# Optimization experiments

Measured on AMD Instinct MI355X. Metric: run time of the kernel, lower is better.

## Reference

```python
import jax, jax.numpy as jnp
import numpy as np

EPS = 1e-7  # K.epsilon()

def setup_inputs() -> dict:
    key = jax.random.key(0)
    k1, k2, k3 = jax.random.split(key, 3)
    B, T, D = 32, 2048, 512
    x = jax.random.normal(k1, (B, T, D), dtype=jnp.float32)
    W = jax.random.normal(k2, (D, D), dtype=jnp.float32) * (1.0 / np.sqrt(D))
    b = jnp.zeros((D,), dtype=jnp.float32)
    u = jax.random.normal(k3, (D,), dtype=jnp.float32) * (1.0 / np.sqrt(D))
    return {"x": x, "W": W, "b": b, "u": u}

def reference(x, W, b, u):
    # uit = tanh(x @ W + b)  -> [B, T, D]
    uit = jnp.tanh(jnp.einsum('btd,de->bte', x, W) + b)
    # scores: sum over feature dim of uit * u -> [B, T]
    ait = jnp.einsum('btd,d->bt', uit, u)
    # exp + normalize over T (no mask); matches original exp/sum form
    a = jnp.exp(ait)
    a = a / (jnp.sum(a, axis=1, keepdims=True) + EPS)
    # weighted sum pooling over T -> [B, D]
    return jnp.einsum('btd,bt->bd', x, a)
```

## Files before the change

kernel.cpp:

```cpp
#include <hip/hip_runtime.h>
#include <math.h>

#define D_DIM 512

typedef short short8v __attribute__((ext_vector_type(8)));
typedef unsigned short ushort8v __attribute__((ext_vector_type(8)));
typedef float f32x16 __attribute__((ext_vector_type(16)));

__device__ inline unsigned short f2bf(float f) {
    union { float f; unsigned int u; } a; a.f = f;
    unsigned int u = a.u;
    unsigned int r = (u + 0x7fffu + ((u >> 16) & 1u)) >> 16;
    return (unsigned short)r;
}

__device__ inline float fast_tanh(float y) {
    float e2 = __expf(2.f * y);
    return 1.f - __fdividef(2.f, e2 + 1.f);
}

#define ASYNC_CP16(gp, lp) \
    __builtin_amdgcn_global_load_lds( \
        (const __attribute__((address_space(1))) void*)(gp), \
        (__attribute__((address_space(3))) void*)(lp), 16, 0, 0)

__global__ __launch_bounds__(1024) void wt_kernel(const float* __restrict__ W,
                                                  unsigned short* __restrict__ Wb2) {
    __shared__ __align__(16) unsigned short lbuf[16384];
    const int s = blockIdx.x;
    const int tid = threadIdx.x;
    #pragma unroll
    for (int i = 0; i < 4; ++i) {
        int flat = tid + i * 1024;
        int kr = flat >> 7;
        int e4 = (flat & 127) * 4;
        float4 v = *(const float4*)(W + (size_t)(s * 32 + kr) * D_DIM + e4);
        int ks = kr >> 4, half = (kr >> 3) & 1, j = kr & 7;
        float vv[4] = {v.x, v.y, v.z, v.w};
        #pragma unroll
        for (int q = 0; q < 4; ++q) {
            int e = e4 + q, nt = e >> 5, nl = e & 31;
            lbuf[(((nt * 2 + ks) * 2 + half) * 32 + nl) * 8 + j] = f2bf(vv[q]);
        }
    }
    __syncthreads();
    #pragma unroll
    for (int i = 0; i < 2; ++i) {
        int c = tid + i * 1024;
        *(ushort8v*)(Wb2 + (size_t)s * 16384 + c * 8) = *(const ushort8v*)&lbuf[c * 8];
    }
}

constexpr int XLDE = 40;

__global__ __launch_bounds__(512, 2) void gemm_ait_mfma(
    const float* __restrict__ x, const unsigned short* __restrict__ Wb2,
    const float* __restrict__ bias, const float* __restrict__ u,
    float* __restrict__ ait)
{
    __shared__ __align__(16) unsigned short wsh[2][16384];
    __shared__ __align__(16) unsigned short xs[2][128 * XLDE];
    __shared__ float rowpart[4][128];

    const int tid  = threadIdx.x;
    const int wave = tid >> 6;
    const int lane = tid & 63;
    const int half = lane >> 5;
    const int nl   = lane & 31;
    const int wr   = wave >> 2;
    const int wc   = wave & 3;
    const int m0   = blockIdx.x * 128;

    f32x16 acc[2][4];
    #pragma unroll
    for (int mi = 0; mi < 2; ++mi)
        #pragma unroll
        for (int ni = 0; ni < 4; ++ni)
            #pragma unroll
            for (int r = 0; r < 16; ++r) acc[mi][ni][r] = 0.f;

    const int xr = tid >> 2;
    const int xc = tid & 3;
    const float* xbase = x + (size_t)(m0 + xr) * D_DIM + xc * 8;

    #pragma unroll
    for (int i = 0; i < 4; ++i)
        ASYNC_CP16(Wb2 + tid * 8 + i * 4096, &wsh[0][tid * 8 + i * 4096]);
    float4 px0 = *(const float4*)(xbase);
    float4 px1 = *(const float4*)(xbase + 4);

    for (int s = 0; s < 16; ++s) {
        const int pb = s & 1;
        {
            ushort8v pk;
            pk[0] = f2bf(px0.x); pk[1] = f2bf(px0.y); pk[2] = f2bf(px0.z); pk[3] = f2bf(px0.w);
            pk[4] = f2bf(px1.x); pk[5] = f2bf(px1.y); pk[6] = f2bf(px1.z); pk[7] = f2bf(px1.w);
            *(ushort8v*)&xs[pb][xr * XLDE + xc * 8] = pk;
        }
        __syncthreads();

        if (s + 1 < 16) {
            const unsigned short* wsrc = Wb2 + (size_t)(s + 1) * 16384;
            #pragma unroll
            for (int i = 0; i < 4; ++i)
                ASYNC_CP16(wsrc + tid * 8 + i * 4096, &wsh[1 - pb][tid * 8 + i * 4096]);
            px0 = *(const float4*)(xbase + (s + 1) * 32);
            px1 = *(const float4*)(xbase + (s + 1) * 32 + 4);
        }

        #pragma unroll
        for (int ks = 0; ks < 2; ++ks) {
            short8v af[2], bfr[4];
            #pragma unroll
            for (int mi = 0; mi < 2; ++mi)
                af[mi] = *(const short8v*)&xs[pb][(wr * 64 + mi * 32 + nl) * XLDE + ks * 16 + half * 8];
            #pragma unroll
            for (int ni = 0; ni < 4; ++ni)
                bfr[ni] = *(const short8v*)&wsh[pb][(((wc * 4 + ni) * 2 + ks) * 2 + half) * 256 + nl * 8];
            #pragma unroll
            for (int mi = 0; mi < 2; ++mi)
                #pragma unroll
                for (int ni = 0; ni < 4; ++ni)
                    acc[mi][ni] = __builtin_amdgcn_mfma_f32_32x32x16_bf16(
                        af[mi], bfr[ni], acc[mi][ni], 0, 0, 0);
        }
    }

    float rowsum[2][16];
    #pragma unroll
    for (int mi = 0; mi < 2; ++mi)
        #pragma unroll
        for (int r = 0; r < 16; ++r) rowsum[mi][r] = 0.f;

    #pragma unroll
    for (int mi = 0; mi < 2; ++mi) {
        #pragma unroll
        for (int ni = 0; ni < 4; ++ni) {
            int col = wc * 128 + ni * 32 + nl;
            float be = bias[col], ue = u[col];
            #pragma unroll
            for (int r = 0; r < 16; ++r)
                rowsum[mi][r] += fast_tanh(acc[mi][ni][r] + be) * ue;
        }
    }
    #pragma unroll
    for (int mi = 0; mi < 2; ++mi)
        #pragma unroll
        for (int r = 0; r < 16; ++r) {
            float v = rowsum[mi][r];
            v += __shfl_xor(v, 1, 64);
            v += __shfl_xor(v, 2, 64);
            v += __shfl_xor(v, 4, 64);
            v += __shfl_xor(v, 8, 64);
            v += __shfl_xor(v, 16, 64);
            rowsum[mi][r] = v;
        }
    if (nl == 0) {
        #pragma unroll
        for (int mi = 0; mi < 2; ++mi)
            #pragma unroll
            for (int r = 0; r < 16; ++r) {
                int row = wr * 64 + mi * 32 + (r & 3) + 8 * (r >> 2) + 4 * half;
                rowpart[wc][row] = rowsum[mi][r];
            }
    }
    __syncthreads();
    if (tid < 128)
        ait[m0 + tid] = rowpart[0][tid] + rowpart[1][tid] + rowpart[2][tid] + rowpart[3][tid];
}

__global__ __launch_bounds__(256) void gemm_ait_f32(
    const float* __restrict__ x, const float* __restrict__ W,
    const float* __restrict__ bias, const float* __restrict__ u,
    float* __restrict__ ait)
{
    __shared__ float xsf[64][68];
    __shared__ float wshf[64][132];
    const int tid = threadIdx.x;
    const int tx = tid & 15, ty = tid >> 4;
    const int m0 = blockIdx.x * 64;
    float rowsum[4] = {0.f, 0.f, 0.f, 0.f};
    for (int e0 = 0; e0 < D_DIM; e0 += 128) {
        float acc[4][8];
        #pragma unroll
        for (int i = 0; i < 4; ++i)
            #pragma unroll
            for (int j = 0; j < 8; ++j) acc[i][j] = 0.f;
        for (int kc = 0; kc < D_DIM; kc += 64) {
            #pragma unroll
            for (int i = 0; i < 4; ++i) {
                int idx = tid + i * 256;
                int r = idx >> 4, c = (idx & 15) * 4;
                *(float4*)&xsf[r][c] = *(const float4*)(x + (size_t)(m0 + r) * D_DIM + kc + c);
            }
            #pragma unroll
            for (int i = 0; i < 8; ++i) {
                int idx = tid + i * 256;
                int r = idx >> 5, c = (idx & 31) * 4;
                *(float4*)&wshf[r][c] = *(const float4*)(W + (size_t)(kc + r) * D_DIM + e0 + c);
            }
            __syncthreads();
            #pragma unroll 4
            for (int k = 0; k < 64; ++k) {
                float xv[4];
                #pragma unroll
                for (int i = 0; i < 4; ++i) xv[i] = xsf[ty * 4 + i][k];
                float4 w0 = *(const float4*)&wshf[k][tx * 8];
                float4 w1 = *(const float4*)&wshf[k][tx * 8 + 4];
                #pragma unroll
                for (int i = 0; i < 4; ++i) {
                    acc[i][0] += xv[i] * w0.x; acc[i][1] += xv[i] * w0.y;
                    acc[i][2] += xv[i] * w0.z; acc[i][3] += xv[i] * w0.w;
                    acc[i][4] += xv[i] * w1.x; acc[i][5] += xv[i] * w1.y;
                    acc[i][6] += xv[i] * w1.z; acc[i][7] += xv[i] * w1.w;
                }
            }
            __syncthreads();
        }
        #pragma unroll
        for (int j = 0; j < 8; ++j) {
            int e = e0 + tx * 8 + j;
            float be = bias[e], ue = u[e];
            #pragma unroll
            for (int i = 0; i < 4; ++i) rowsum[i] += tanhf(acc[i][j] + be) * ue;
        }
    }
    float* red = &xsf[0][0];
    #pragma unroll
    for (int i = 0; i < 4; ++i) red[(ty * 4 + i) * 16 + tx] = rowsum[i];
    __syncthreads();
    if (tid < 64) {
        float s = 0.f;
        #pragma unroll
        for (int j = 0; j < 16; ++j) s += red[tid * 16 + j];
        ait[m0 + tid] = s;
    }
}

__global__ __launch_bounds__(256) void softmax_kernel(float* __restrict__ ait, int T)
{
    const int b = blockIdx.x;
    float* p = ait + (size_t)b * T;
    const int tid = threadIdx.x;
    float ev[8];
    float local = 0.f;
    #pragma unroll
    for (int i = 0; i < 8; ++i) {
        ev[i] = expf(p[tid + i * 256]);
        local += ev[i];
    }
    #pragma unroll
    for (int off = 32; off > 0; off >>= 1)
        local += __shfl_down(local, off, 64);
    __shared__ float wsum[4];
    const int wv = tid >> 6, lane = tid & 63;
    if (lane == 0) wsum[wv] = local;
    __syncthreads();
    float total = wsum[0] + wsum[1] + wsum[2] + wsum[3];
    float inv = 1.0f / (total + 1e-7f);
    #pragma unroll
    for (int i = 0; i < 8; ++i) p[tid + i * 256] = ev[i] * inv;
}

__global__ __launch_bounds__(256) void pool_partial_kernel(
    const float* __restrict__ x, const float* __restrict__ a,
    float* __restrict__ partial, int T)
{
    const int chunks = T >> 8;
    const int b = blockIdx.x / chunks;
    const int c = blockIdx.x % chunks;
    const int tid = threadIdx.x;
    const int th = tid >> 7;
    const int d = (tid & 127) * 4;

    const float* xp = x + ((size_t)b * T + c * 256) * D_DIM + d;
    const float* ap = a + (size_t)b * T + c * 256;

    float4 acc = {0.f, 0.f, 0.f, 0.f};
    #pragma unroll 8
    for (int t = th; t < 256; t += 2) {
        float s = ap[t];
        float4 xv = *(const float4*)(xp + (size_t)t * D_DIM);
        acc.x += xv.x * s; acc.y += xv.y * s;
        acc.z += xv.z * s; acc.w += xv.w * s;
    }
    __shared__ float4 tmp[128];
    if (th == 1) tmp[tid & 127] = acc;
    __syncthreads();
    if (th == 0) {
        float4 o = tmp[tid];
        acc.x += o.x; acc.y += o.y; acc.z += o.z; acc.w += o.w;
        *(float4*)(partial + (size_t)blockIdx.x * D_DIM + tid * 4) = acc;
    }
}

__global__ __launch_bounds__(256) void pool_reduce_kernel(
    const float* __restrict__ partial, float* __restrict__ out, int chunks)
{
    const int b = blockIdx.x;
    const int tid = threadIdx.x;
    const int d = tid * 2;
    float2 acc = {0.f, 0.f};
    for (int c = 0; c < chunks; ++c) {
        float2 v = *(const float2*)(partial + ((size_t)b * chunks + c) * D_DIM + d);
        acc.x += v.x; acc.y += v.y;
    }
    *(float2*)(out + (size_t)b * D_DIM + d) = acc;
}

__global__ __launch_bounds__(256) void pool_atomic_kernel(
    const float* __restrict__ x, const float* __restrict__ a,
    float* __restrict__ out, int T)
{
    const int chunks = T >> 8;
    const int b = blockIdx.x / chunks;
    const int c = blockIdx.x % chunks;
    const int tid = threadIdx.x;
    const int th = tid >> 7;
    const int d = (tid & 127) * 4;
    const float* xp = x + ((size_t)b * T + c * 256) * D_DIM + d;
    const float* ap = a + (size_t)b * T + c * 256;
    float4 acc = {0.f, 0.f, 0.f, 0.f};
    #pragma unroll 8
    for (int t = th; t < 256; t += 2) {
        float s = ap[t];
        float4 xv = *(const float4*)(xp + (size_t)t * D_DIM);
        acc.x += xv.x * s; acc.y += xv.y * s;
        acc.z += xv.z * s; acc.w += xv.w * s;
    }
    __shared__ float4 tmp[128];
    if (th == 1) tmp[tid & 127] = acc;
    __syncthreads();
    if (th == 0) {
        float4 o = tmp[tid];
        float* op = out + (size_t)b * D_DIM + tid * 4;
        atomicAdd(op + 0, acc.x + o.x);
        atomicAdd(op + 1, acc.y + o.y);
        atomicAdd(op + 2, acc.z + o.z);
        atomicAdd(op + 3, acc.w + o.w);
    }
}

extern "C" void kernel_launch(void* const* d_in, const int* in_sizes, int n_in,
                              void* d_out, int out_size, void* d_ws, size_t ws_size,
                              hipStream_t stream)
{
    const float* x    = (const float*)d_in[0];
    const float* W    = (const float*)d_in[1];
    const float* bias = (const float*)d_in[2];
    const float* u    = (const float*)d_in[3];
    float* out = (float*)d_out;

    const int Dd = in_sizes[2];
    const int M  = in_sizes[0] / Dd;
    const int B  = out_size / Dd;
    const int T  = M / B;
    const int chunks = T >> 8;

    const size_t wb_bytes  = (size_t)Dd * Dd * sizeof(unsigned short);
    const size_t ait_bytes = (size_t)M * sizeof(float);

    if (ws_size >= wb_bytes + ait_bytes) {
        unsigned short* Wb2 = (unsigned short*)d_ws;
        float* ait     = (float*)((char*)d_ws + wb_bytes);
        float* partial = (float*)d_ws;

        wt_kernel<<<dim3(16), dim3(1024), 0, stream>>>(W, Wb2);
        gemm_ait_mfma<<<dim3(M / 128), dim3(512), 0, stream>>>(x, Wb2, bias, u, ait);
        softmax_kernel<<<dim3(B), dim3(256), 0, stream>>>(ait, T);
        pool_partial_kernel<<<dim3(B * chunks), dim3(256), 0, stream>>>(x, ait, partial, T);
        pool_reduce_kernel<<<dim3(B), dim3(256), 0, stream>>>(partial, out, chunks);
    } else {
        float* ait = (float*)d_ws;
        gemm_ait_f32<<<dim3(M / 64), dim3(256), 0, stream>>>(x, W, bias, u, ait);
        softmax_kernel<<<dim3(B), dim3(256), 0, stream>>>(ait, T);
        hipMemsetAsync(d_out, 0, (size_t)out_size * sizeof(float), stream);
        pool_atomic_kernel<<<dim3(B * chunks), dim3(256), 0, stream>>>(x, ait, out, T);
    }
}
```

Measured before the change: 262.4 us.

## Shrink GEMM row tile to 64 and widen pooling blocks to 512 threads

The scoring GEMM now handles 64 rows per block instead of 128, and each of the 8 waves owns a 64-column slice across all rows. The launch bound now asks for 4 blocks per CU, and the grid doubles. The pooling partial kernel uses 512 threads, with four time-strided groups reduced through shared memory, for more memory parallelism. The smaller tile raises occupancy, but every block must still load the full W, so W traffic from LDS and L2 per row doubles.

```diff
diff --git a/kernel.cpp b/kernel.cpp
--- a/kernel.cpp
+++ b/kernel.cpp
@@ -5,6 +5,7 @@
 
 typedef short short8v __attribute__((ext_vector_type(8)));
 typedef unsigned short ushort8v __attribute__((ext_vector_type(8)));
+typedef unsigned short ushort4v __attribute__((ext_vector_type(4)));
 typedef float f32x16 __attribute__((ext_vector_type(16)));
 
 __device__ inline unsigned short f2bf(float f) {
@@ -53,49 +54,46 @@
 
 constexpr int XLDE = 40;
 
-__global__ __launch_bounds__(512, 2) void gemm_ait_mfma(
+__global__ __launch_bounds__(512, 4) void gemm_ait_mfma(
     const float* __restrict__ x, const unsigned short* __restrict__ Wb2,
     const float* __restrict__ bias, const float* __restrict__ u,
     float* __restrict__ ait)
 {
     __shared__ __align__(16) unsigned short wsh[2][16384];
-    __shared__ __align__(16) unsigned short xs[2][128 * XLDE];
-    __shared__ float rowpart[4][128];
+    __shared__ __align__(16) unsigned short xs[2][64 * XLDE];
+    __shared__ float rowpart[8][64];
 
     const int tid  = threadIdx.x;
     const int wave = tid >> 6;
     const int lane = tid & 63;
     const int half = lane >> 5;
     const int nl   = lane & 31;
-    const int wr   = wave >> 2;
-    const int wc   = wave & 3;
-    const int m0   = blockIdx.x * 128;
-
-    f32x16 acc[2][4];
+    const int m0   = blockIdx.x * 64;
+
+    f32x16 acc[2][2];
     #pragma unroll
     for (int mi = 0; mi < 2; ++mi)
         #pragma unroll
-        for (int ni = 0; ni < 4; ++ni)
+        for (int ni = 0; ni < 2; ++ni)
             #pragma unroll
             for (int r = 0; r < 16; ++r) acc[mi][ni][r] = 0.f;
 
-    const int xr = tid >> 2;
-    const int xc = tid & 3;
-    const float* xbase = x + (size_t)(m0 + xr) * D_DIM + xc * 8;
+    const int xr  = tid >> 3;
+    const int xc4 = tid & 7;
+    const float* xbase = x + (size_t)(m0 + xr) * D_DIM + xc4 * 4;
 
     #pragma unroll
     for (int i = 0; i < 4; ++i)
         ASYNC_CP16(Wb2 + tid * 8 + i * 4096, &wsh[0][tid * 8 + i * 4096]);
-    float4 px0 = *(const float4*)(xbase);
-    float4 px1 = *(const float4*)(xbase + 4);
+    float4 px = *(const float4*)(xbase);
 
     for (int s = 0; s < 16; ++s) {
         const int pb = s & 1;
         {
-            ushort8v pk;
-            pk[0] = f2bf(px0.x); pk[1] = f2bf(px0.y); pk[2] = f2bf(px0.z); pk[3] = f2bf(px0.w);
-            pk[4] = f2bf(px1.x); pk[5] = f2bf(px1.y); pk[6] = f2bf(px1.z); pk[7] = f2bf(px1.w);
-            *(ushort8v*)&xs[pb][xr * XLDE + xc * 8] = pk;
+            ushort4v pk;
+            pk[0] = f2bf(px.x); pk[1] = f2bf(px.y);
+            pk[2] = f2bf(px.z); pk[3] = f2bf(px.w);
+            *(ushort4v*)&xs[pb][xr * XLDE + xc4 * 4] = pk;
         }
         __syncthreads();
 
@@ -104,23 +102,22 @@
             #pragma unroll
             for (int i = 0; i < 4; ++i)
                 ASYNC_CP16(wsrc + tid * 8 + i * 4096, &wsh[1 - pb][tid * 8 + i * 4096]);
-            px0 = *(const float4*)(xbase + (s + 1) * 32);
-            px1 = *(const float4*)(xbase + (s + 1) * 32 + 4);
+            px = *(const float4*)(xbase + (s + 1) * 32);
         }
 
         #pragma unroll
         for (int ks = 0; ks < 2; ++ks) {
-            short8v af[2], bfr[4];
+            short8v af[2], bfr[2];
             #pragma unroll
             for (int mi = 0; mi < 2; ++mi)
-                af[mi] = *(const short8v*)&xs[pb][(wr * 64 + mi * 32 + nl) * XLDE + ks * 16 + half * 8];
-            #pragma unroll
-            for (int ni = 0; ni < 4; ++ni)
-                bfr[ni] = *(const short8v*)&wsh[pb][(((wc * 4 + ni) * 2 + ks) * 2 + half) * 256 + nl * 8];
+                af[mi] = *(const short8v*)&xs[pb][(mi * 32 + nl) * XLDE + ks * 16 + half * 8];
+            #pragma unroll
+            for (int ni = 0; ni < 2; ++ni)
+                bfr[ni] = *(const short8v*)&wsh[pb][(((wave * 2 + ni) * 2 + ks) * 2 + half) * 256 + nl * 8];
             #pragma unroll
             for (int mi = 0; mi < 2; ++mi)
                 #pragma unroll
-                for (int ni = 0; ni < 4; ++ni)
+                for (int ni = 0; ni < 2; ++ni)
                     acc[mi][ni] = __builtin_amdgcn_mfma_f32_32x32x16_bf16(
                         af[mi], bfr[ni], acc[mi][ni], 0, 0, 0);
         }
@@ -135,8 +132,8 @@
     #pragma unroll
     for (int mi = 0; mi < 2; ++mi) {
         #pragma unroll
-        for (int ni = 0; ni < 4; ++ni) {
-            int col = wc * 128 + ni * 32 + nl;
+        for (int ni = 0; ni < 2; ++ni) {
+            int col = wave * 64 + ni * 32 + nl;
             float be = bias[col], ue = u[col];
             #pragma unroll
             for (int r = 0; r < 16; ++r)
@@ -160,13 +157,17 @@
         for (int mi = 0; mi < 2; ++mi)
             #pragma unroll
             for (int r = 0; r < 16; ++r) {
-                int row = wr * 64 + mi * 32 + (r & 3) + 8 * (r >> 2) + 4 * half;
-                rowpart[wc][row] = rowsum[mi][r];
+                int row = mi * 32 + (r & 3) + 8 * (r >> 2) + 4 * half;
+                rowpart[wave][row] = rowsum[mi][r];
             }
     }
     __syncthreads();
-    if (tid < 128)
-        ait[m0 + tid] = rowpart[0][tid] + rowpart[1][tid] + rowpart[2][tid] + rowpart[3][tid];
+    if (tid < 64) {
+        float s = 0.f;
+        #pragma unroll
+        for (int w = 0; w < 8; ++w) s += rowpart[w][tid];
+        ait[m0 + tid] = s;
+    }
 }
 
 __global__ __launch_bounds__(256) void gemm_ait_f32(
@@ -262,7 +263,7 @@
     for (int i = 0; i < 8; ++i) p[tid + i * 256] = ev[i] * inv;
 }
 
-__global__ __launch_bounds__(256) void pool_partial_kernel(
+__global__ __launch_bounds__(512) void pool_partial_kernel(
     const float* __restrict__ x, const float* __restrict__ a,
     float* __restrict__ partial, int T)
 {
@@ -278,18 +279,19 @@
 
     float4 acc = {0.f, 0.f, 0.f, 0.f};
     #pragma unroll 8
-    for (int t = th; t < 256; t += 2) {
+    for (int t = th; t < 256; t += 4) {
         float s = ap[t];
         float4 xv = *(const float4*)(xp + (size_t)t * D_DIM);
         acc.x += xv.x * s; acc.y += xv.y * s;
         acc.z += xv.z * s; acc.w += xv.w * s;
     }
-    __shared__ float4 tmp[128];
-    if (th == 1) tmp[tid & 127] = acc;
+    __shared__ float4 tmp[3][128];
+    if (th > 0) tmp[th - 1][tid & 127] = acc;
     __syncthreads();
     if (th == 0) {
-        float4 o = tmp[tid];
-        acc.x += o.x; acc.y += o.y; acc.z += o.z; acc.w += o.w;
+        float4 o0 = tmp[0][tid], o1 = tmp[1][tid], o2 = tmp[2][tid];
+        acc.x += o0.x + o1.x + o2.x; acc.y += o0.y + o1.y + o2.y;
+        acc.z += o0.z + o1.z + o2.z; acc.w += o0.w + o1.w + o2.w;
         *(float4*)(partial + (size_t)blockIdx.x * D_DIM + tid * 4) = acc;
     }
 }
@@ -366,9 +368,9 @@
         float* partial = (float*)d_ws;
 
         wt_kernel<<<dim3(16), dim3(1024), 0, stream>>>(W, Wb2);
-        gemm_ait_mfma<<<dim3(M / 128), dim3(512), 0, stream>>>(x, Wb2, bias, u, ait);
+        gemm_ait_mfma<<<dim3(M / 64), dim3(512), 0, stream>>>(x, Wb2, bias, u, ait);
         softmax_kernel<<<dim3(B), dim3(256), 0, stream>>>(ait, T);
-        pool_partial_kernel<<<dim3(B * chunks), dim3(256), 0, stream>>>(x, ait, partial, T);
+        pool_partial_kernel<<<dim3(B * chunks), dim3(512), 0, stream>>>(x, ait, partial, T);
         pool_reduce_kernel<<<dim3(B), dim3(256), 0, stream>>>(partial, out, chunks);
     } else {
         float* ait = (float*)d_ws;
```

Measured after the change: 256.6 us. 2.2% less time.
